# Optimization experiments

Hardware: AMD Instinct MI355X
Metric: run time of the kernel (lower is better)

The kernel has to match this reference:

```python
import math
import jax, jax.numpy as jnp
import numpy as np

B, S, D, H, HD = 2, 2048, 1024, 16, 64  # batch, seq, dim, heads, head_dim
EPS = 1e-5

def setup_inputs() -> dict:
    key = jax.random.key(0)
    ks = jax.random.split(key, 10)
    init = lambda k, shape: jax.random.normal(k, shape, jnp.float32) * 0.02
    return {
        "x": jax.random.normal(ks[0], (B, S, D), jnp.float32),
        "cos": jax.random.uniform(ks[1], (1, S, 1, 1, HD), dtype=jnp.float32),
        "sin": jax.random.uniform(ks[2], (1, S, 1, 1, HD), dtype=jnp.float32),
        "c": jax.random.normal(ks[3], (B, D), jnp.float32),
        "norm1_w": jnp.ones((D,), jnp.float32),
        "w_qkv": init(ks[4], (3 * D, D)),
        "w_out": init(ks[5], (D, D)),
        "norm2_w": jnp.ones((D,), jnp.float32),
        "mlp_w1": init(ks[6], (4 * D, D)),
        "mlp_b1": jnp.zeros((4 * D,), jnp.float32),
        "mlp_w2": init(ks[7], (D, 4 * D)),
        "mlp_b2": jnp.zeros((D,), jnp.float32),
        "ada_w": init(ks[8], (6 * D, D)),
        "ada_b": init(ks[9], (6 * D,)),
    }

def _ln(x, w):
    # LayerNorm computed in fp32, no bias, then scaled by weight
    xf = x.astype(jnp.float32)
    mu = xf.mean(-1, keepdims=True)
    var = xf.var(-1, keepdims=True)
    return (xf - mu) * jax.lax.rsqrt(var + EPS) * w

def _modulate(h, shift, scale):
    return h * (1.0 + scale[:, None, :]) + shift[:, None, :]

def reference(x, cos, sin, c, norm1_w, w_qkv, w_out, norm2_w,
              mlp_w1, mlp_b1, mlp_w2, mlp_b2, ada_w, ada_b):
    # adaLN modulation params: [B, 6D] -> six [B, D] chunks
    ada = c @ ada_w.T + ada_b
    sh_msa, sc_msa, g_msa, sh_mlp, sc_mlp, g_mlp = jnp.split(ada, 6, axis=-1)

    # attention branch (flash_attn path: no rotary applied, naive full softmax)
    h = _modulate(_ln(x, norm1_w), sh_msa, sc_msa)
    qkv = (h @ w_qkv.T).reshape(B, S, 3, H, HD)
    q, k, v = qkv[:, :, 0], qkv[:, :, 1], qkv[:, :, 2]
    scores = jnp.einsum('bqhd,bkhd->bhqk', q, k) / math.sqrt(HD)
    probs = jax.nn.softmax(scores, axis=-1)
    attn = jnp.einsum('bhqk,bkhd->bqhd', probs, v).reshape(B, S, D)
    # gate * dropout(out) + residual; eval mode -> dropout = identity
    x = x + g_msa[:, None, :] * (attn @ w_out.T)

    # MLP branch
    h = _modulate(_ln(x, norm2_w), sh_mlp, sc_mlp)
    h = jax.nn.gelu(h @ mlp_w1.T + mlp_b1, approximate=True) @ mlp_w2.T + mlp_b2
    return x + g_mlp[:, None, :] * h
```

## Files before the change

kernel.cpp:

```cpp
#include <hip/hip_runtime.h>
#include <stdint.h>

typedef __attribute__((ext_vector_type(4))) float f32x4;
typedef __attribute__((ext_vector_type(8))) __bf16 bf16x8;

#define DEV static __device__ __forceinline__

DEV unsigned short f2bf(float f){
    uint32_t u = __float_as_uint(f);
    u += 0x7FFFu + ((u >> 16) & 1u);
    return (unsigned short)(u >> 16);
}
DEV uint32_t pk2bf(float a, float b){
    return (uint32_t)f2bf(a) | ((uint32_t)f2bf(b) << 16);
}

#define GLDS16(g, l) __builtin_amdgcn_global_load_lds( \
    (const __attribute__((address_space(1))) void*)(g), \
    (__attribute__((address_space(3))) void*)(l), 16, 0, 0)

__global__ __launch_bounds__(256) void k_cast_bf16(const float* __restrict__ in,
                                                   unsigned short* __restrict__ out, int n4){
    int i = blockIdx.x * 256 + threadIdx.x;
    if (i < n4){
        float4 v = ((const float4*)in)[i];
        ((ushort4*)out)[i] = make_ushort4(f2bf(v.x), f2bf(v.y), f2bf(v.z), f2bf(v.w));
    }
}

__global__ __launch_bounds__(256) void k_ada(const float* __restrict__ c,
                                             const float* __restrict__ aw,
                                             const float* __restrict__ ab,
                                             float* __restrict__ out){
    int wid  = blockIdx.x * 4 + (threadIdx.x >> 6);
    int lane = threadIdx.x & 63;
    int b = wid / 6144, r = wid % 6144;
    const float4* cw = (const float4*)(c + (size_t)b * 1024);
    const float4* wr = (const float4*)(aw + (size_t)r * 1024);
    float s = 0.f;
    #pragma unroll
    for (int i = 0; i < 4; i++){
        float4 a = wr[lane + i * 64];
        float4 q = cw[lane + i * 64];
        s += a.x*q.x + a.y*q.y + a.z*q.z + a.w*q.w;
    }
    #pragma unroll
    for (int off = 32; off > 0; off >>= 1) s += __shfl_down(s, off);
    if (lane == 0) out[wid] = s + ab[r];
}

__global__ __launch_bounds__(256) void k_ln_mod(const float* __restrict__ x,
                                                const float* __restrict__ w,
                                                const float* __restrict__ ada,
                                                int sh_off, int sc_off,
                                                unsigned short* __restrict__ out){
    int row = blockIdx.x;
    int b   = row >> 11;
    int tid = threadIdx.x;
    float4 v = ((const float4*)(x + (size_t)row * 1024))[tid];
    float s  = v.x + v.y + v.z + v.w;
    float ss = v.x*v.x + v.y*v.y + v.z*v.z + v.w*v.w;
    #pragma unroll
    for (int off = 32; off > 0; off >>= 1){ s += __shfl_down(s, off); ss += __shfl_down(ss, off); }
    __shared__ float red[8];
    int wv = tid >> 6;
    if ((tid & 63) == 0){ red[wv] = s; red[4 + wv] = ss; }
    __syncthreads();
    float S  = red[0] + red[1] + red[2] + red[3];
    float SS = red[4] + red[5] + red[6] + red[7];
    float mu   = S * (1.f / 1024.f);
    float rstd = rsqrtf(SS * (1.f / 1024.f) - mu * mu + 1e-5f);
    const float* adab = ada + (size_t)b * 6144;
    float4 wv4 = ((const float4*)w)[tid];
    float4 sh  = ((const float4*)(adab + sh_off))[tid];
    float4 sc  = ((const float4*)(adab + sc_off))[tid];
    float h0 = (v.x - mu) * rstd * wv4.x * (1.f + sc.x) + sh.x;
    float h1 = (v.y - mu) * rstd * wv4.y * (1.f + sc.y) + sh.y;
    float h2 = (v.z - mu) * rstd * wv4.z * (1.f + sc.z) + sh.z;
    float h3 = (v.w - mu) * rstd * wv4.w * (1.f + sc.w) + sh.w;
    ((ushort4*)(out + (size_t)row * 1024))[tid] = make_ushort4(f2bf(h0), f2bf(h1), f2bf(h2), f2bf(h3));
}

template<int MODE, int BM>
__global__ __launch_bounds__(256) void k_gemm(const unsigned short* __restrict__ A,
                                              const unsigned short* __restrict__ B,
                                              void* __restrict__ outp,
                                              const float* __restrict__ bias,
                                              const float* __restrict__ res,
                                              const float* __restrict__ ada, int goff,
                                              int M, int N, int K){
    constexpr int NT = (BM == 128) ? 4 : 2;
    constexpr int NW = NT * 16;
    __shared__ unsigned short As[BM * 32];
    __shared__ unsigned short Bs[128 * 32];
    int tid = threadIdx.x, lane = tid & 63, wv = tid >> 6;
    int quad = lane >> 4, l15 = lane & 15;
    int wm = (BM == 128) ? (wv & 1) : 0;
    int wn = (BM == 128) ? (wv >> 1) : wv;
    int bm = blockIdx.x, bn = blockIdx.y;
    f32x4 acc[4][NT] = {};
    const unsigned short* ga = A + (size_t)(bm * BM + wv * 16 + (lane >> 2)) * K + (lane & 3) * 8;
    const unsigned short* gb = B + (size_t)(bn * 128 + wv * 16 + (lane >> 2)) * K + (lane & 3) * 8;
    size_t stride64 = (size_t)64 * K;
    unsigned short* la0 = As + wv * 16 * 32;
    unsigned short* la1 = As + (wv * 16 + 64) * 32;
    unsigned short* lb0 = Bs + wv * 16 * 32;
    unsigned short* lb1 = Bs + (wv * 16 + 64) * 32;
    for (int k0 = 0; k0 < K; k0 += 32){
        __syncthreads();
        GLDS16(ga + k0, la0);
        if constexpr (BM == 128) GLDS16(ga + stride64 + k0, la1);
        GLDS16(gb + k0, lb0);
        GLDS16(gb + stride64 + k0, lb1);
        __syncthreads();
        bf16x8 af[4], bfr[NT];
        #pragma unroll
        for (int i = 0; i < 4; i++)
            af[i] = *(const bf16x8*)(As + (wm * 64 + i * 16 + l15) * 32 + quad * 8);
        #pragma unroll
        for (int j = 0; j < NT; j++)
            bfr[j] = *(const bf16x8*)(Bs + (wn * NW + j * 16 + l15) * 32 + quad * 8);
        #pragma unroll
        for (int i = 0; i < 4; i++)
            #pragma unroll
            for (int j = 0; j < NT; j++)
                acc[i][j] = __builtin_amdgcn_mfma_f32_16x16x32_bf16(af[i], bfr[j], acc[i][j], 0, 0, 0);
    }
    int row0 = bm * BM + wm * 64, col0 = bn * 128 + wn * NW;
    #pragma unroll
    for (int i = 0; i < 4; i++){
        #pragma unroll
        for (int r = 0; r < 4; r++){
            int row = row0 + i * 16 + quad * 4 + r;
            #pragma unroll
            for (int j = 0; j < NT; j++){
                int col = col0 + j * 16 + l15;
                float v = acc[i][j][r];
                size_t idx = (size_t)row * N + col;
                if constexpr (MODE == 0){
                    ((unsigned short*)outp)[idx] = f2bf(v);
                } else if constexpr (MODE == 1){
                    float t = v + bias[col];
                    float u = 0.7978845608028654f * (t + 0.044715f * t * t * t);
                    float g = 0.5f * t * (1.f + tanhf(u));
                    ((unsigned short*)outp)[idx] = f2bf(g);
                } else {
                    float t = v;
                    if (bias) t += bias[col];
                    int bb = row >> 11;
                    float g = ada[(size_t)bb * 6144 + goff + col];
                    ((float*)outp)[idx] = res[idx] + g * t;
                }
            }
        }
    }
}

__global__ __launch_bounds__(256) void k_vt(const unsigned short* __restrict__ qkv,
                                            unsigned short* __restrict__ vt){
    __shared__ unsigned short T[64 * 66];
    int kb = blockIdx.x, bh = blockIdx.y;
    int b = bh >> 4, h = bh & 15;
    size_t rb = (size_t)b * 2048;
    int t = threadIdx.x;
    int key = t >> 2, seg = t & 3;
    const unsigned short* src = qkv + (rb + kb * 64 + key) * 3072 + 2048 + h * 64;
    uint4 v0 = *(const uint4*)(src + seg * 8);
    uint4 v1 = *(const uint4*)(src + 32 + seg * 8);
    const unsigned short* p0 = (const unsigned short*)&v0;
    const unsigned short* p1 = (const unsigned short*)&v1;
    unsigned short* tr = T + key * 66;
    ushort2* t0 = (ushort2*)(tr + seg * 8);
    ushort2* t1 = (ushort2*)(tr + 32 + seg * 8);
    #pragma unroll
    for (int j = 0; j < 4; j++){
        t0[j] = make_ushort2(p0[2*j], p0[2*j+1]);
        t1[j] = make_ushort2(p1[2*j], p1[2*j+1]);
    }
    __syncthreads();
    int d = t >> 2, kseg = t & 3;
    unsigned short obuf[16];
    #pragma unroll
    for (int j = 0; j < 16; j++) obuf[j] = T[(kseg * 16 + j) * 66 + d];
    uint4* dst = (uint4*)(vt + ((size_t)bh * 64 + d) * 2048 + kb * 64 + kseg * 16);
    dst[0] = ((const uint4*)obuf)[0];
    dst[1] = ((const uint4*)obuf)[1];
}

__global__ __launch_bounds__(256) void k_attn(const unsigned short* __restrict__ qkv,
                                              const unsigned short* __restrict__ vt,
                                              unsigned short* __restrict__ out){
    __shared__ unsigned short Ks[2 * 64 * 32];
    __shared__ unsigned short Vs[2 * 64 * 32];
    __shared__ __align__(16) unsigned short Ps[4 * 32 * 72];
    int tid = threadIdx.x, lane = tid & 63, wv = tid >> 6;
    int quad = lane >> 4, l15 = lane & 15;
    int qt = blockIdx.x, bh = blockIdx.y;
    int b = bh >> 4, h = bh & 15;
    size_t rb = (size_t)b * 2048;

    bf16x8 qb[2][2];
    #pragma unroll
    for (int t = 0; t < 2; t++){
        int qrow = qt * 128 + wv * 32 + t * 16 + l15;
        const unsigned short* qp = qkv + ((rb + qrow) * 3072 + h * 64 + quad * 8);
        qb[t][0] = *(const bf16x8*)qp;
        qb[t][1] = *(const bf16x8*)(qp + 32);
    }
    float lsum[2] = {0.f, 0.f};
    f32x4 o[2][4];
    #pragma unroll
    for (int t = 0; t < 2; t++)
        #pragma unroll
        for (int dt = 0; dt < 4; dt++) o[t][dt] = (f32x4){0.f, 0.f, 0.f, 0.f};

    int rr = wv * 16 + (lane >> 2), cs = lane & 3;
    const unsigned short* gk = qkv + (rb + rr) * 3072 + 1024 + h * 64 + cs * 8;
    const unsigned short* gv = vt + ((size_t)bh * 64 + rr) * 2048 + cs * 8;
    unsigned short* lk0 = Ks + wv * 16 * 32;
    unsigned short* lk1 = Ks + 2048 + wv * 16 * 32;
    unsigned short* lv0 = Vs + wv * 16 * 32;
    unsigned short* lv1 = Vs + 2048 + wv * 16 * 32;
    unsigned short* Pw = Ps + wv * 32 * 72;

    for (int k0 = 0; k0 < 2048; k0 += 64){
        __syncthreads();
        GLDS16(gk + (size_t)k0 * 3072,      lk0);
        GLDS16(gk + (size_t)k0 * 3072 + 32, lk1);
        GLDS16(gv + k0,      lv0);
        GLDS16(gv + k0 + 32, lv1);
        __syncthreads();
        f32x4 c[2][4];
        #pragma unroll
        for (int kt = 0; kt < 4; kt++){
            bf16x8 ka0 = *(const bf16x8*)(Ks + (kt * 16 + l15) * 32 + quad * 8);
            bf16x8 ka1 = *(const bf16x8*)(Ks + 2048 + (kt * 16 + l15) * 32 + quad * 8);
            #pragma unroll
            for (int t = 0; t < 2; t++){
                f32x4 z = (f32x4){0.f, 0.f, 0.f, 0.f};
                z = __builtin_amdgcn_mfma_f32_16x16x32_bf16(ka0, qb[t][0], z, 0, 0, 0);
                z = __builtin_amdgcn_mfma_f32_16x16x32_bf16(ka1, qb[t][1], z, 0, 0, 0);
                c[t][kt] = z;
            }
        }
        #pragma unroll
        for (int t = 0; t < 2; t++){
            #pragma unroll
            for (int kt = 0; kt < 4; kt++){
                float p0 = __expf(c[t][kt][0] * 0.125f);
                float p1 = __expf(c[t][kt][1] * 0.125f);
                float p2 = __expf(c[t][kt][2] * 0.125f);
                float p3 = __expf(c[t][kt][3] * 0.125f);
                lsum[t] += (p0 + p1) + (p2 + p3);
                uint2 w;
                w.x = pk2bf(p0, p1);
                w.y = pk2bf(p2, p3);
                *(uint2*)(Pw + (t * 16 + l15) * 72 + kt * 16 + quad * 4) = w;
            }
        }
        bf16x8 pa[2][2];
        #pragma unroll
        for (int t = 0; t < 2; t++){
            pa[t][0] = *(const bf16x8*)(Pw + (t * 16 + l15) * 72 + quad * 8);
            pa[t][1] = *(const bf16x8*)(Pw + (t * 16 + l15) * 72 + 32 + quad * 8);
        }
        #pragma unroll
        for (int dt = 0; dt < 4; dt++){
            bf16x8 vb0 = *(const bf16x8*)(Vs + (dt * 16 + l15) * 32 + quad * 8);
            bf16x8 vb1 = *(const bf16x8*)(Vs + 2048 + (dt * 16 + l15) * 32 + quad * 8);
            #pragma unroll
            for (int t = 0; t < 2; t++){
                o[t][dt] = __builtin_amdgcn_mfma_f32_16x16x32_bf16(pa[t][0], vb0, o[t][dt], 0, 0, 0);
                o[t][dt] = __builtin_amdgcn_mfma_f32_16x16x32_bf16(pa[t][1], vb1, o[t][dt], 0, 0, 0);
            }
        }
    }
    #pragma unroll
    for (int t = 0; t < 2; t++){
        lsum[t] += __shfl_xor(lsum[t], 16);
        lsum[t] += __shfl_xor(lsum[t], 32);
    }
    #pragma unroll
    for (int t = 0; t < 2; t++){
        #pragma unroll
        for (int r = 0; r < 4; r++){
            float lt = __shfl(lsum[t], quad * 4 + r);
            float inv = 1.f / lt;
            int row = qt * 128 + wv * 32 + t * 16 + quad * 4 + r;
            unsigned short* op = out + ((rb + row) * 1024 + h * 64);
            #pragma unroll
            for (int dt = 0; dt < 4; dt++)
                op[dt * 16 + l15] = f2bf(o[t][dt][r] * inv);
        }
    }
}

extern "C" void kernel_launch(void* const* d_in, const int* in_sizes, int n_in,
                              void* d_out, int out_size, void* d_ws, size_t ws_size,
                              hipStream_t stream){
    const float* x     = (const float*)d_in[0];
    const float* c     = (const float*)d_in[3];
    const float* n1w   = (const float*)d_in[4];
    const float* w_qkv = (const float*)d_in[5];
    const float* w_out = (const float*)d_in[6];
    const float* n2w   = (const float*)d_in[7];
    const float* w1    = (const float*)d_in[8];
    const float* b1    = (const float*)d_in[9];
    const float* w2    = (const float*)d_in[10];
    const float* b2    = (const float*)d_in[11];
    const float* ada_w = (const float*)d_in[12];
    const float* ada_b = (const float*)d_in[13];
    float* out = (float*)d_out;
    char* ws = (char*)d_ws;

    unsigned short* wqkv_b = (unsigned short*)(ws + 0);
    unsigned short* wout_b = (unsigned short*)(ws + 6291456);
    unsigned short* w1_b   = (unsigned short*)(ws + 8388608);
    unsigned short* w2_b   = (unsigned short*)(ws + 16777216);
    float*          ada    = (float*)         (ws + 25165824);
    unsigned short* h      = (unsigned short*)(ws + 25214976);
    unsigned short* qkv    = (unsigned short*)(ws + 33603584);
    unsigned short* attn   = (unsigned short*)(ws + 58769408);
    float*          xn     = (float*)         (ws + 67158016);
    unsigned short* u      = qkv;
    unsigned short* vt     = h;

    k_cast_bf16<<<3072, 256, 0, stream>>>(w_qkv, wqkv_b,  786432);
    k_cast_bf16<<<1024, 256, 0, stream>>>(w_out, wout_b,  262144);
    k_cast_bf16<<<4096, 256, 0, stream>>>(w1,    w1_b,   1048576);
    k_cast_bf16<<<4096, 256, 0, stream>>>(w2,    w2_b,   1048576);
    k_ada<<<3072, 256, 0, stream>>>(c, ada_w, ada_b, ada);
    k_ln_mod<<<4096, 256, 0, stream>>>(x, n1w, ada, 0, 1024, h);
    k_gemm<0,128><<<dim3(32, 24), 256, 0, stream>>>(h, wqkv_b, qkv, nullptr, nullptr, nullptr, 0, 4096, 3072, 1024);
    k_vt<<<dim3(32, 32), 256, 0, stream>>>(qkv, vt);
    k_attn<<<dim3(16, 32), 256, 0, stream>>>(qkv, vt, attn);
    k_gemm<2,64><<<dim3(64, 8), 256, 0, stream>>>(attn, wout_b, xn, nullptr, x, ada, 2048, 4096, 1024, 1024);
    k_ln_mod<<<4096, 256, 0, stream>>>(xn, n2w, ada, 3072, 4096, h);
    k_gemm<1,128><<<dim3(32, 32), 256, 0, stream>>>(h, w1_b, u, b1, nullptr, nullptr, 0, 4096, 4096, 1024);
    k_gemm<2,64><<<dim3(64, 8), 256, 0, stream>>>(u, w2_b, out, b2, xn, ada, 5120, 4096, 1024, 4096);
}
```

Baseline: 453.0 us.

## Split-K the MLP down-projection GEMM with atomic accumulation and separate epilogue

The final MLP down-projection (K=4096) now runs as a 4-way split-K GEMM with 128-row tiles. Each split atomically adds fp32 partial sums into a zeroed workspace buffer. A new elementwise kernel then applies bias, the adaLN gate and the residual. The aim is more blocks with shorter K loops for better CU occupancy and larger tiles for more reuse. The cost is a memset, fp32 atomic traffic, an extra epilogue pass, and a workspace buffer that aliases the already-consumed bf16 weight copies.

Result: slower. 476.9 us (+5.3%).

```diff
diff --git a/kernel.cpp b/kernel.cpp
--- a/kernel.cpp
+++ b/kernel.cpp
@@ -98,6 +98,8 @@
     int wm = (BM == 128) ? (wv & 1) : 0;
     int wn = (BM == 128) ? (wv >> 1) : wv;
     int bm = blockIdx.x, bn = blockIdx.y;
+    int kpb = K / gridDim.z;
+    int klo = blockIdx.z * kpb, khi = klo + kpb;
     f32x4 acc[4][NT] = {};
     const unsigned short* ga = A + (size_t)(bm * BM + wv * 16 + (lane >> 2)) * K + (lane & 3) * 8;
     const unsigned short* gb = B + (size_t)(bn * 128 + wv * 16 + (lane >> 2)) * K + (lane & 3) * 8;
@@ -106,7 +108,7 @@
     unsigned short* la1 = As + (wv * 16 + 64) * 32;
     unsigned short* lb0 = Bs + wv * 16 * 32;
     unsigned short* lb1 = Bs + (wv * 16 + 64) * 32;
-    for (int k0 = 0; k0 < K; k0 += 32){
+    for (int k0 = klo; k0 < khi; k0 += 32){
         __syncthreads();
         GLDS16(ga + k0, la0);
         if constexpr (BM == 128) GLDS16(ga + stride64 + k0, la1);
@@ -144,16 +146,40 @@
                     float u = 0.7978845608028654f * (t + 0.044715f * t * t * t);
                     float g = 0.5f * t * (1.f + tanhf(u));
                     ((unsigned short*)outp)[idx] = f2bf(g);
-                } else {
+                } else if constexpr (MODE == 2){
                     float t = v;
                     if (bias) t += bias[col];
                     int bb = row >> 11;
                     float g = ada[(size_t)bb * 6144 + goff + col];
                     ((float*)outp)[idx] = res[idx] + g * t;
+                } else {
+                    unsafeAtomicAdd((float*)outp + idx, v);
                 }
             }
         }
     }
+}
+
+__global__ __launch_bounds__(256) void k_ep(const float* __restrict__ acc,
+                                            const float* __restrict__ bias,
+                                            const float* __restrict__ res,
+                                            const float* __restrict__ ada, int goff,
+                                            float* __restrict__ out, int N){
+    int row = blockIdx.x;
+    int bb  = row >> 11;
+    int tid = threadIdx.x;
+    const float* adag = ada + (size_t)bb * 6144 + goff;
+    size_t base = (size_t)row * N;
+    float4 a = ((const float4*)(acc + base))[tid];
+    float4 rv = ((const float4*)(res + base))[tid];
+    float4 bv = ((const float4*)bias)[tid];
+    float4 gv = ((const float4*)adag)[tid];
+    float4 o;
+    o.x = rv.x + gv.x * (a.x + bv.x);
+    o.y = rv.y + gv.y * (a.y + bv.y);
+    o.z = rv.z + gv.z * (a.z + bv.z);
+    o.w = rv.w + gv.w * (a.w + bv.w);
+    ((float4*)(out + base))[tid] = o;
 }
 
 __global__ __launch_bounds__(256) void k_vt(const unsigned short* __restrict__ qkv,
@@ -324,6 +350,7 @@
     float*          xn     = (float*)         (ws + 67158016);
     unsigned short* u      = qkv;
     unsigned short* vt     = h;
+    float*          accb   = (float*)ws;
 
     k_cast_bf16<<<3072, 256, 0, stream>>>(w_qkv, wqkv_b,  786432);
     k_cast_bf16<<<1024, 256, 0, stream>>>(w_out, wout_b,  262144);
@@ -337,5 +364,7 @@
     k_gemm<2,64><<<dim3(64, 8), 256, 0, stream>>>(attn, wout_b, xn, nullptr, x, ada, 2048, 4096, 1024, 1024);
     k_ln_mod<<<4096, 256, 0, stream>>>(xn, n2w, ada, 3072, 4096, h);
     k_gemm<1,128><<<dim3(32, 32), 256, 0, stream>>>(h, w1_b, u, b1, nullptr, nullptr, 0, 4096, 4096, 1024);
-    k_gemm<2,64><<<dim3(64, 8), 256, 0, stream>>>(u, w2_b, out, b2, xn, ada, 5120, 4096, 1024, 4096);
-}
+    hipMemsetAsync(accb, 0, 16777216, stream);
+    k_gemm<3,128><<<dim3(32, 8, 4), 256, 0, stream>>>(u, w2_b, accb, nullptr, nullptr, nullptr, 0, 4096, 1024, 4096);
+    k_ep<<<4096, 256, 0, stream>>>(accb, b2, xn, ada, 5120, out, 1024);
+}
```
